# Performance work log

Hardware: AMD Instinct MI355X
Metric: run time of the kernel (lower is better)

The kernel has to match this reference:

```python
import jax, jax.numpy as jnp
import numpy as np
import math

V, H, NH, L, S, B = 100000, 2048, 64, 2, 512, 2
HD = H // NH  # 32
MAX_LEN = 5000
EPS_NORM = 1e-5
EPS_ATTN = 1e-6


def build_pe():
    # PositionalEncoding buffer: pe[max_len, 1, d_model]
    position = jnp.arange(MAX_LEN, dtype=jnp.float32)[:, None]
    div_term = jnp.exp(jnp.arange(0, H, 2, dtype=jnp.float32) * (-math.log(10000.0) / H))
    ang = position * div_term  # [max_len, H/2]
    pe = jnp.zeros((MAX_LEN, 1, H), dtype=jnp.float32)
    pe = pe.at[:, 0, 0::2].set(jnp.sin(ang))
    pe = pe.at[:, 0, 1::2].set(jnp.cos(ang))
    return pe


def fast_inv_sqrt(x):
    # Quake fast inverse sqrt; the bit-trick seed is detached in the original
    x2 = x * 0.5
    i = jax.lax.bitcast_convert_type(jax.lax.stop_gradient(x.astype(jnp.float32)), jnp.int32)
    i = jnp.int32(1597463007) - (i >> 1)
    y = jax.lax.bitcast_convert_type(i, jnp.float32)
    return y * (1.5 - x2 * y * y)  # grad flows only through x2, as in torch


def sr_norm(h, w, b):
    mean = h.mean(-1, keepdims=True)
    var = ((h - mean) ** 2).mean(-1, keepdims=True)  # biased variance
    inv = fast_inv_sqrt(var + EPS_NORM)
    return w * ((h - mean) * inv) + b


def attn_layer(x, wq, bq, wk, bk, wv, bv, wo, bo, nw, nb):
    # x: [B, S, H]; weights stored [in, out]
    def heads(t):
        return t.reshape(B, S, NH, HD).transpose(0, 2, 1, 3)  # [B, NH, S, HD]
    q = heads(x @ wq + bq)
    k = heads(x @ wk + bk)
    v = heads(x @ wv + bv)
    scores = jnp.einsum('bhqd,bhkd->bhqk', q, k) / math.sqrt(HD)
    a = jax.nn.softmax(scores, axis=-1)
    # dropout is identity in eval; then double softmax (exp/sum) + sigmoid gate
    e = jnp.exp(a)
    a2 = e / (e.sum(-1, keepdims=True) + EPS_ATTN)
    cw = a2 * jax.nn.sigmoid(a2)
    o = jnp.einsum('bhqk,bhkd->bhqd', cw, v)
    o = o.transpose(0, 2, 1, 3).reshape(B, S, H)
    o = o @ wo + bo
    return sr_norm(o + x, nw, nb)


def setup_inputs():
    key = jax.random.key(0)
    ks = jax.random.split(key, 12)
    def rn(k, shape):
        return jax.random.normal(k, shape, dtype=jnp.float32) * 0.02
    return {
        'src': jax.random.randint(ks[0], (B, S), 0, V),
        'emb': jax.random.uniform(ks[1], (V, H), minval=-0.1, maxval=0.1, dtype=jnp.float32),
        'Wq': rn(ks[2], (L, H, H)), 'bq': jnp.zeros((L, H), jnp.float32),
        'Wk': rn(ks[3], (L, H, H)), 'bk': jnp.zeros((L, H), jnp.float32),
        'Wv': rn(ks[4], (L, H, H)), 'bv': jnp.zeros((L, H), jnp.float32),
        'Wo': rn(ks[5], (L, H, H)), 'bo': jnp.zeros((L, H), jnp.float32),
        'nw': jnp.ones((L, H), jnp.float32), 'nb': jnp.zeros((L, H), jnp.float32),
        'Wout': jax.random.uniform(ks[6], (H, V), minval=-0.1, maxval=0.1, dtype=jnp.float32),
        'bout': jnp.zeros((V,), jnp.float32),
    }


def reference(src, emb, Wq, bq, Wk, bk, Wv, bv, Wo, bo, nw, nb, Wout, bout):
    x = emb[src] * math.sqrt(H)  # [B, S, H]
    pe = build_pe()
    # Faithful to pe[:x.size(0)] where x is [B, S, H]: indexes by BATCH dim
    x = x + pe[:x.shape[0]]  # [B, 1, H] broadcast over seq
    for l in range(L):
        x = attn_layer(x, Wq[l], bq[l], Wk[l], bk[l], Wv[l], bv[l],
                       Wo[l], bo[l], nw[l], nb[l])
    return x @ Wout + bout  # [B, S, V]
```

## Files before the change

### kernel.cpp

```cpp
#include <hip/hip_runtime.h>


#define DEVINL __device__ __forceinline__

typedef float f32x4 __attribute__((ext_vector_type(4)));
typedef __bf16 bf16x8 __attribute__((ext_vector_type(8)));
typedef __bf16 bf16x2v __attribute__((ext_vector_type(2)));

DEVINL unsigned int pk2(float a, float b) {
  bf16x2v v;
  v[0] = (__bf16)a;
  v[1] = (__bf16)b;
  return __builtin_bit_cast(unsigned int, v);
}

DEVINL void gload_lds16(const void* g, void* l) {
  __builtin_amdgcn_global_load_lds(
      (const __attribute__((address_space(1))) unsigned int*)g,
      (__attribute__((address_space(3))) unsigned int*)l, 16, 0, 0);
}

__global__ __launch_bounds__(256) void peinit_kernel(float* __restrict__ pe_tab) {
  const int h = blockIdx.x * 256 + threadIdx.x;
  const float c = -9.210340371976184f / 2048.f;
  const int i = h >> 1;
  const float dv = expf((float)(2 * i) * c);
#pragma unroll
  for (int b = 0; b < 2; ++b) {
    float ang = (float)b * dv;
    pe_tab[b * 2048 + h] = (h & 1) ? cosf(ang) : sinf(ang);
  }
}

__global__ __launch_bounds__(256) void embed_kernel(
    const int* __restrict__ src, const float* __restrict__ emb,
    const float* __restrict__ pe_tab, float* __restrict__ x, unsigned short* __restrict__ xbf) {
  const int row = blockIdx.x;
  const int b = row >> 9;
  const int tok = src[row];
  const float sqrtH = 45.25483399593904f;
  const float* er = emb + (size_t)tok * 2048;
  const float* pr = pe_tab + b * 2048;
  for (int c0 = threadIdx.x * 4; c0 < 2048; c0 += 1024) {
    float4 e = *(const float4*)(er + c0);
    float4 p = *(const float4*)(pr + c0);
    float r0 = fmaf(e.x, sqrtH, p.x), r1 = fmaf(e.y, sqrtH, p.y);
    float r2 = fmaf(e.z, sqrtH, p.z), r3 = fmaf(e.w, sqrtH, p.w);
    *(float4*)(x + (size_t)row * 2048 + c0) = make_float4(r0, r1, r2, r3);
    *(uint2*)&xbf[(size_t)row * 2048 + c0] = make_uint2(pk2(r0, r1), pk2(r2, r3));
  }
}

__global__ __launch_bounds__(256) void wtrans_kernel(
    const float* __restrict__ W, unsigned short* __restrict__ WT, const int N) {
  __shared__ float t[64][65];
  const int tid = threadIdx.x;
  const int n0 = blockIdx.x * 64, k0 = blockIdx.y * 64;
  const int c4 = (tid & 15) * 4;
#pragma unroll
  for (int it = 0; it < 4; ++it) {
    int kl = it * 16 + (tid >> 4);
    int n = n0 + c4;
    float4 wv;
    if (n + 3 < N) {
      wv = *(const float4*)(W + (size_t)(k0 + kl) * N + n);
    } else {
      wv.x = (n + 0 < N) ? W[(size_t)(k0 + kl) * N + n + 0] : 0.f;
      wv.y = (n + 1 < N) ? W[(size_t)(k0 + kl) * N + n + 1] : 0.f;
      wv.z = (n + 2 < N) ? W[(size_t)(k0 + kl) * N + n + 2] : 0.f;
      wv.w = (n + 3 < N) ? W[(size_t)(k0 + kl) * N + n + 3] : 0.f;
    }
    t[kl][c4 + 0] = wv.x;
    t[kl][c4 + 1] = wv.y;
    t[kl][c4 + 2] = wv.z;
    t[kl][c4 + 3] = wv.w;
  }
  __syncthreads();
  const int kp = (tid & 7) * 8;
#pragma unroll
  for (int j = 0; j < 2; ++j) {
    int nl = j * 32 + (tid >> 3);
    uint4 u;
    u.x = pk2(t[kp + 0][nl], t[kp + 1][nl]);
    u.y = pk2(t[kp + 2][nl], t[kp + 3][nl]);
    u.z = pk2(t[kp + 4][nl], t[kp + 5][nl]);
    u.w = pk2(t[kp + 6][nl], t[kp + 7][nl]);
    *(uint4*)&WT[(size_t)(n0 + nl) * 2048 + k0 + kp] = u;
  }
}

template <int BM, int NN>
DEVINL void gemm_bf_body(const unsigned short* __restrict__ A,
                         const unsigned short* __restrict__ BT,
                         const float* __restrict__ bias, float* __restrict__ C,
                         const int m0, const int n0) {
  constexpr int K = 2048;
  constexpr int NT = K / 32;
  constexpr int WM = BM / 32;
  constexpr int LP = BM / 64 + 2;
  __shared__ __align__(16) unsigned short A_lds[3][BM * 32];
  __shared__ __align__(16) unsigned short B_lds[3][128 * 32];

  const int tid = threadIdx.x;
  const int w = tid >> 6, lane = tid & 63;
  const int wm = w >> 1, wn = w & 1;

  const int aRow = lane >> 2;
  const int aChunk = (lane & 3) ^ ((lane >> 3) & 3);

  int aOff[WM], bOff[4];
#pragma unroll
  for (int mi = 0; mi < WM; ++mi) {
    int m = wm * (BM / 2) + mi * 16 + (lane & 15);
    aOff[mi] = m * 32 + ((lane >> 4) ^ ((m >> 1) & 3)) * 8;
  }
#pragma unroll
  for (int ni = 0; ni < 4; ++ni) {
    int n = wn * 64 + ni * 16 + (lane & 15);
    bOff[ni] = n * 32 + ((lane >> 4) ^ ((n >> 1) & 3)) * 8;
  }

  f32x4 acc[WM][4] = {};

  auto stage = [&](int k0, int bf) {
#pragma unroll
    for (int i = 0; i < BM / 64; ++i) {
      int r0 = (w * (BM / 64) + i) * 16;
      gload_lds16(A + (size_t)(m0 + r0 + aRow) * K + k0 + aChunk * 8, &A_lds[bf][r0 * 32]);
    }
#pragma unroll
    for (int i = 0; i < 2; ++i) {
      int r0 = (w * 2 + i) * 16;
      gload_lds16(BT + (size_t)(n0 + r0 + aRow) * K + k0 + aChunk * 8, &B_lds[bf][r0 * 32]);
    }
  };
  auto compute = [&](int bf) {
    bf16x8 af[WM], bfr[4];
#pragma unroll
    for (int mi = 0; mi < WM; ++mi) af[mi] = *(const bf16x8*)&A_lds[bf][aOff[mi]];
#pragma unroll
    for (int ni = 0; ni < 4; ++ni) bfr[ni] = *(const bf16x8*)&B_lds[bf][bOff[ni]];
#pragma unroll
    for (int mi = 0; mi < WM; ++mi)
#pragma unroll
      for (int ni = 0; ni < 4; ++ni)
        acc[mi][ni] = __builtin_amdgcn_mfma_f32_16x16x32_bf16(af[mi], bfr[ni], acc[mi][ni], 0, 0, 0);
  };

  stage(0, 0);
  stage(32, 1);
  for (int t = 0; t < NT - 1; ++t) {
    asm volatile("s_waitcnt vmcnt(%0)" :: "i"(LP) : "memory");
    __builtin_amdgcn_s_barrier();
    if (t < NT - 2) stage((t + 2) * 32, (t + 2) % 3);
    compute(t % 3);
  }
  asm volatile("s_waitcnt vmcnt(0)" ::: "memory");
  __builtin_amdgcn_s_barrier();
  compute((NT - 1) % 3);

  const int r0w = (lane >> 4) * 4;
  const int lrow = lane & 15;
#pragma unroll
  for (int mi = 0; mi < WM; ++mi)
#pragma unroll
    for (int ni = 0; ni < 4; ++ni) {
      int ccol = n0 + wn * 64 + ni * 16 + lrow;
      if ((NN % 128 == 0) || ccol < NN) {
        float bv = bias[ccol];
#pragma unroll
        for (int r = 0; r < 4; ++r) {
          int crow = m0 + wm * (BM / 2) + mi * 16 + r0w + r;
          C[(size_t)crow * NN + ccol] = acc[mi][ni][r] + bv;
        }
      }
    }
}

template <int BM, int NN>
__global__ __launch_bounds__(256) void gemm_bf_kernel(
    const unsigned short* __restrict__ A, const unsigned short* __restrict__ BT,
    const float* __restrict__ bias, float* __restrict__ C) {
  gemm_bf_body<BM, NN>(A, BT, bias, C, blockIdx.x * BM, blockIdx.y * 128);
}

__global__ __launch_bounds__(256) void gemm_qkv_bf_kernel(
    const unsigned short* __restrict__ A, const unsigned short* __restrict__ WT,
    const float* __restrict__ bq, const float* __restrict__ bk, const float* __restrict__ bv,
    float* __restrict__ q, float* __restrict__ k, float* __restrict__ v) {
  const int z = blockIdx.z;
  const unsigned short* BT = WT + (size_t)z * 2048 * 2048;
  const float* bias = (z == 0) ? bq : (z == 1) ? bk : bv;
  float* C = (z == 0) ? q : (z == 1) ? k : v;
  gemm_bf_body<128, 2048>(A, BT, bias, C, blockIdx.x * 128, blockIdx.y * 128);
}

__global__ __launch_bounds__(256) void gemm_final_bf_kernel(
    const unsigned short* __restrict__ A, const unsigned short* __restrict__ BT,
    const float* __restrict__ bias, float* __restrict__ C) {
  const int bid = blockIdx.x;
  const int f = (bid & 7) * (gridDim.x >> 3) + (bid >> 3);
  gemm_bf_body<128, 100000>(A, BT, bias, C, (f & 7) * 128, (f >> 3) * 128);
}

template <int BM>
DEVINL void gemm_body(const unsigned short* __restrict__ A, const float* __restrict__ B,
                      const float* __restrict__ bias, float* __restrict__ C,
                      const int N, const int m0, const int n0) {
  constexpr int K = 2048;
  constexpr int WM = BM / 32;
  constexpr int AI = BM / 64;
  __shared__ __align__(16) unsigned short A_lds[2][BM * 32];
  __shared__ __align__(16) unsigned short B_lds[2][128 * 32];

  const int tid = threadIdx.x;
  const int w = tid >> 6, lane = tid & 63;
  const int wm = w >> 1, wn = w & 1;

  const int n_local = tid & 127;
  const int kq = tid >> 7;
  const int col = n0 + n_local;
  const bool colok = col < N;
  const int bswz = (n_local >> 1) & 3;

  const int aRow = lane >> 2;
  const int aChunk = (lane & 3) ^ ((lane >> 3) & 3);

  int aOff[WM], bOff[4];
#pragma unroll
  for (int mi = 0; mi < WM; ++mi) {
    int m = wm * (BM / 2) + mi * 16 + (lane & 15);
    aOff[mi] = m * 32 + ((lane >> 4) ^ ((m >> 1) & 3)) * 8;
  }
#pragma unroll
  for (int ni = 0; ni < 4; ++ni) {
    int n = wn * 64 + ni * 16 + (lane & 15);
    bOff[ni] = n * 32 + ((lane >> 4) ^ ((n >> 1) & 3)) * 8;
  }

  f32x4 acc[WM][4] = {};
  float fB[16];

  auto stageA = [&](int k0, int bf) {
#pragma unroll
    for (int i = 0; i < AI; ++i) {
      int r0 = (w * AI + i) * 16;
      gload_lds16(A + (size_t)(m0 + r0 + aRow) * K + k0 + aChunk * 8, &A_lds[bf][r0 * 32]);
    }
  };
  auto loadB = [&](int k0) {
#pragma unroll
    for (int g = 0; g < 4; ++g) {
      int kl = (g * 2 + kq) * 4;
#pragma unroll
      for (int i = 0; i < 4; ++i)
        fB[g * 4 + i] = colok ? B[(size_t)(k0 + kl + i) * N + col] : 0.f;
    }
  };
  auto writeB = [&](int bf) {
#pragma unroll
    for (int g = 0; g < 4; ++g) {
      int kl = (g * 2 + kq) * 4;
      uint2 p = make_uint2(pk2(fB[g * 4 + 0], fB[g * 4 + 1]),
                           pk2(fB[g * 4 + 2], fB[g * 4 + 3]));
      int chunk = (kl >> 3) ^ bswz;
      *(uint2*)&B_lds[bf][n_local * 32 + chunk * 8 + (kl & 7)] = p;
    }
  };
  auto compute = [&](int bf) {
    bf16x8 af[WM], bfr[4];
#pragma unroll
    for (int mi = 0; mi < WM; ++mi) af[mi] = *(const bf16x8*)&A_lds[bf][aOff[mi]];
#pragma unroll
    for (int ni = 0; ni < 4; ++ni) bfr[ni] = *(const bf16x8*)&B_lds[bf][bOff[ni]];
#pragma unroll
    for (int mi = 0; mi < WM; ++mi)
#pragma unroll
      for (int ni = 0; ni < 4; ++ni)
        acc[mi][ni] = __builtin_amdgcn_mfma_f32_16x16x32_bf16(af[mi], bfr[ni], acc[mi][ni], 0, 0, 0);
  };

  stageA(0, 0);
  loadB(0);
  writeB(0);
  __syncthreads();
  int buf = 0;
  for (int t = 0; t < K / 32 - 1; ++t) {
    stageA((t + 1) * 32, buf ^ 1);
    loadB((t + 1) * 32);
    compute(buf);
    writeB(buf ^ 1);
    __syncthreads();
    buf ^= 1;
  }
  compute(buf);

  const int r0w = (lane >> 4) * 4;
  const int lrow = lane & 15;
#pragma unroll
  for (int mi = 0; mi < WM; ++mi)
#pragma unroll
    for (int ni = 0; ni < 4; ++ni) {
      int ccol = n0 + wn * 64 + ni * 16 + lrow;
      if (ccol < N) {
        float bv = bias[ccol];
#pragma unroll
        for (int r = 0; r < 4; ++r) {
          int crow = m0 + wm * (BM / 2) + mi * 16 + r0w + r;
          C[(size_t)crow * N + ccol] = acc[mi][ni][r] + bv;
        }
      }
    }
}

__global__ __launch_bounds__(256) void gemm_qkv_kernel(
    const unsigned short* __restrict__ A,
    const float* __restrict__ Wq, const float* __restrict__ Wk, const float* __restrict__ Wv,
    const float* __restrict__ bq, const float* __restrict__ bk, const float* __restrict__ bv,
    float* __restrict__ q, float* __restrict__ k, float* __restrict__ v) {
  const int z = blockIdx.z;
  const float* B = (z == 0) ? Wq : (z == 1) ? Wk : Wv;
  const float* bias = (z == 0) ? bq : (z == 1) ? bk : bv;
  float* C = (z == 0) ? q : (z == 1) ? k : v;
  gemm_body<64>(A, B, bias, C, 2048, blockIdx.x * 64, blockIdx.y * 128);
}

template <int BM>
__global__ __launch_bounds__(256) void gemm_kernel(
    const unsigned short* __restrict__ A, const float* __restrict__ B,
    const float* __restrict__ bias, float* __restrict__ C, const int N) {
  gemm_body<BM>(A, B, bias, C, N, blockIdx.x * BM, blockIdx.y * 128);
}

__global__ __launch_bounds__(256) void gemm_final_kernel(
    const unsigned short* __restrict__ A, const float* __restrict__ B,
    const float* __restrict__ bias, float* __restrict__ C, const int N) {
  const int bid = blockIdx.x;
  const int f = (bid & 7) * (gridDim.x >> 3) + (bid >> 3);
  gemm_body<128>(A, B, bias, C, N, (f & 7) * 128, (f >> 3) * 128);
}

__global__ __launch_bounds__(256) void attn_kernel(
    const float* __restrict__ q, const float* __restrict__ k,
    const float* __restrict__ v, unsigned short* __restrict__ o) {
  __shared__ __align__(16) float K_lds[512 * 32];
  const int tid = threadIdx.x;
  const int blk = blockIdx.x;
  const int bh = blk >> 2, chunk = blk & 3;
  const int b = bh >> 6, h = bh & 63;
  const size_t headoff = (size_t)b * 512 * 2048 + (size_t)h * 32;

  const float* kb = k + headoff;
#pragma unroll
  for (int i = 0; i < 16; ++i) {
    int flat = i * 256 + tid;
    int j = flat >> 3, d4 = flat & 7;
    *(float4*)&K_lds[j * 32 + d4 * 4] = *(const float4*)(kb + (size_t)j * 2048 + d4 * 4);
  }
  __syncthreads();

  const int row = chunk * 128 + (tid >> 1);
  const int half = tid & 1;
  const int j0 = half * 256, j1 = j0 + 256;
  const float* qr = q + headoff + (size_t)row * 2048;
  float4 Q[8];
#pragma unroll
  for (int d = 0; d < 8; ++d) Q[d] = *(const float4*)(qr + d * 4);

  const float scale = 0.17677669529663689f;
  auto dot = [&](int j) -> float {
    const float4* kr = (const float4*)&K_lds[j * 32];
    float p0 = 0.f, p1 = 0.f, p2 = 0.f, p3 = 0.f;
#pragma unroll
    for (int d = 0; d < 8; ++d) {
      float4 kk = kr[d];
      p0 = fmaf(Q[d].x, kk.x, p0);
      p1 = fmaf(Q[d].y, kk.y, p1);
      p2 = fmaf(Q[d].z, kk.z, p2);
      p3 = fmaf(Q[d].w, kk.w, p3);
    }
    return ((p0 + p1) + (p2 + p3)) * scale;
  };

  float m = -1e30f, denom = 0.f;
  for (int j = j0; j < j1; ++j) {
    float s = dot(j);
    float nm = fmaxf(m, s);
    denom = denom * __expf(m - nm) + __expf(s - nm);
    m = nm;
  }
  {
    float m2 = __shfl_xor(m, 1);
    float d2 = __shfl_xor(denom, 1);
    float mm = fmaxf(m, m2);
    denom = denom * __expf(m - mm) + d2 * __expf(m2 - mm);
    m = mm;
  }
  const float invd = 1.f / denom;

  float sum_e = 0.f;
  for (int j = j0; j < j1; ++j) {
    float a = __expf(dot(j) - m) * invd;
    sum_e += __expf(a);
  }
  sum_e += __shfl_xor(sum_e, 1);
  const float inv_se = 1.f / (sum_e + 1e-6f);

  float4 accv[8];
#pragma unroll
  for (int d = 0; d < 8; ++d) accv[d] = make_float4(0.f, 0.f, 0.f, 0.f);
  const float* vb = v + headoff;
  float4 vcur[8];
#pragma unroll
  for (int d = 0; d < 8; ++d) vcur[d] = *(const float4*)(vb + (size_t)j0 * 2048 + d * 4);
  for (int j = j0; j < j1; ++j) {
    float4 vnxt[8];
    if (j + 1 < j1) {
      const float4* vr = (const float4*)(vb + (size_t)(j + 1) * 2048);
#pragma unroll
      for (int d = 0; d < 8; ++d) vnxt[d] = vr[d];
    } else {
#pragma unroll
      for (int d = 0; d < 8; ++d) vnxt[d] = vcur[d];
    }
    float a = __expf(dot(j) - m) * invd;
    float e = __expf(a);
    float a2 = e * inv_se;
    float cw = a2 / (1.f + __expf(-a2));
#pragma unroll
    for (int d = 0; d < 8; ++d) {
      accv[d].x = fmaf(cw, vcur[d].x, accv[d].x);
      accv[d].y = fmaf(cw, vcur[d].y, accv[d].y);
      accv[d].z = fmaf(cw, vcur[d].z, accv[d].z);
      accv[d].w = fmaf(cw, vcur[d].w, accv[d].w);
    }
#pragma unroll
    for (int d = 0; d < 8; ++d) vcur[d] = vnxt[d];
  }
#pragma unroll
  for (int d = 0; d < 8; ++d) {
    accv[d].x += __shfl_xor(accv[d].x, 1);
    accv[d].y += __shfl_xor(accv[d].y, 1);
    accv[d].z += __shfl_xor(accv[d].z, 1);
    accv[d].w += __shfl_xor(accv[d].w, 1);
  }
  unsigned short* orow = o + headoff + (size_t)row * 2048;
#pragma unroll
  for (int g = 0; g < 4; ++g) {
    int d = half * 4 + g;
    uint2 p = make_uint2(pk2(accv[d].x, accv[d].y), pk2(accv[d].z, accv[d].w));
    *(uint2*)&orow[d * 4] = p;
  }
}

__global__ __launch_bounds__(256) void norm_kernel(
    const float* __restrict__ o, const float* __restrict__ xin,
    const float* __restrict__ w, const float* __restrict__ bb,
    float* __restrict__ xout, unsigned short* __restrict__ xbf) {
  __shared__ float red[4];
  const int row = blockIdx.x, tid = threadIdx.x;
  const float* op = o + (size_t)row * 2048;
  const float* xp = xin + (size_t)row * 2048;
  float4 hv[2];
#pragma unroll
  for (int i = 0; i < 2; ++i) {
    float4 a = *(const float4*)(op + tid * 4 + i * 1024);
    float4 c = *(const float4*)(xp + tid * 4 + i * 1024);
    hv[i] = make_float4(a.x + c.x, a.y + c.y, a.z + c.z, a.w + c.w);
  }
  float s = 0.f;
#pragma unroll
  for (int i = 0; i < 2; ++i) s += hv[i].x + hv[i].y + hv[i].z + hv[i].w;
  for (int off = 32; off; off >>= 1) s += __shfl_down(s, off);
  if ((tid & 63) == 0) red[tid >> 6] = s;
  __syncthreads();
  const float mean = (red[0] + red[1] + red[2] + red[3]) * (1.f / 2048.f);
  __syncthreads();

  float vs = 0.f;
#pragma unroll
  for (int i = 0; i < 2; ++i) {
    float dx = hv[i].x - mean, dy = hv[i].y - mean, dz = hv[i].z - mean, dw = hv[i].w - mean;
    vs += dx * dx + dy * dy + dz * dz + dw * dw;
  }
  for (int off = 32; off; off >>= 1) vs += __shfl_down(vs, off);
  if ((tid & 63) == 0) red[tid >> 6] = vs;
  __syncthreads();
  const float var = (red[0] + red[1] + red[2] + red[3]) * (1.f / 2048.f);

  const float xv = var + 1e-5f;
  int ii = __float_as_int(xv);
  ii = 1597463007 - (ii >> 1);
  float y = __int_as_float(ii);
  y = y * (1.5f - 0.5f * xv * y * y);

#pragma unroll
  for (int i = 0; i < 2; ++i) {
    int c0 = tid * 4 + i * 1024;
    float4 wv = *(const float4*)(w + c0);
    float4 bv = *(const float4*)(bb + c0);
    float r0 = wv.x * ((hv[i].x - mean) * y) + bv.x;
    float r1 = wv.y * ((hv[i].y - mean) * y) + bv.y;
    float r2 = wv.z * ((hv[i].z - mean) * y) + bv.z;
    float r3 = wv.w * ((hv[i].w - mean) * y) + bv.w;
    *(float4*)(xout + (size_t)row * 2048 + c0) = make_float4(r0, r1, r2, r3);
    *(uint2*)&xbf[(size_t)row * 2048 + c0] = make_uint2(pk2(r0, r1), pk2(r2, r3));
  }
}

extern "C" void kernel_launch(void* const* d_in, const int* in_sizes, int n_in,
                              void* d_out, int out_size, void* d_ws, size_t ws_size,
                              hipStream_t stream) {
  const int*   src  = (const int*)d_in[0];
  const float* emb  = (const float*)d_in[1];
  const float* Wq   = (const float*)d_in[2];
  const float* bq   = (const float*)d_in[3];
  const float* Wk   = (const float*)d_in[4];
  const float* bk   = (const float*)d_in[5];
  const float* Wv   = (const float*)d_in[6];
  const float* bv   = (const float*)d_in[7];
  const float* Wo   = (const float*)d_in[8];
  const float* bo   = (const float*)d_in[9];
  const float* nw   = (const float*)d_in[10];
  const float* nb   = (const float*)d_in[11];
  const float* Wout = (const float*)d_in[12];
  const float* bout = (const float*)d_in[13];
  float* out = (float*)d_out;

  char* ws = (char*)d_ws;
  float* x  = (float*)(ws);
  float* qb = (float*)(ws + (8ll << 20));
  float* kb = (float*)(ws + (16ll << 20));
  float* vb = (float*)(ws + (24ll << 20));
  float* ob = (float*)(ws + (32ll << 20));
  unsigned short* xbf = (unsigned short*)(ws + (40ll << 20));
  unsigned short* abf = (unsigned short*)(ws + (44ll << 20));
  float* pe_tab = ob;

  const unsigned long long NEED = (112ull << 20) + 100096ull * 2048ull * 2ull;
  const bool big = (unsigned long long)ws_size >= NEED;
  unsigned short* WTp = (unsigned short*)(ws + (48ll << 20));
  unsigned short* WTo = (unsigned short*)(ws + (112ll << 20));

  peinit_kernel<<<8, 256, 0, stream>>>(pe_tab);
  embed_kernel<<<1024, 256, 0, stream>>>(src, emb, pe_tab, x, xbf);

  if (big) {
    for (int l = 0; l < 2; ++l) {
      const size_t wo_ = (size_t)l * 2048 * 2048;
      const float* Wm[4] = {Wq + wo_, Wk + wo_, Wv + wo_, Wo + wo_};
      for (int mt = 0; mt < 4; ++mt)
        wtrans_kernel<<<dim3(32, 32), 256, 0, stream>>>(
            Wm[mt], WTp + (size_t)(l * 4 + mt) * 2048 * 2048, 2048);
    }
    wtrans_kernel<<<dim3(1564, 32), 256, 0, stream>>>(Wout, WTo, 100000);

    for (int l = 0; l < 2; ++l) {
      const size_t bo_ = (size_t)l * 2048;
      const unsigned short* WTl = WTp + (size_t)(l * 4) * 2048 * 2048;
      gemm_qkv_bf_kernel<<<dim3(8, 16, 3), 256, 0, stream>>>(
          xbf, WTl, bq + bo_, bk + bo_, bv + bo_, qb, kb, vb);
      attn_kernel<<<512, 256, 0, stream>>>(qb, kb, vb, abf);
      gemm_bf_kernel<64, 2048><<<dim3(16, 16), 256, 0, stream>>>(
          abf, WTl + (size_t)3 * 2048 * 2048, bo + bo_, ob);
      norm_kernel<<<1024, 256, 0, stream>>>(ob, x, nw + bo_, nb + bo_, x, xbf);
    }
    gemm_final_bf_kernel<<<8 * 782, 256, 0, stream>>>(xbf, WTo, bout, out);
  } else {
    for (int l = 0; l < 2; ++l) {
      const size_t wo_ = (size_t)l * 2048 * 2048;
      const size_t bo_ = (size_t)l * 2048;
      gemm_qkv_kernel<<<dim3(16, 16, 3), 256, 0, stream>>>(
          xbf, Wq + wo_, Wk + wo_, Wv + wo_, bq + bo_, bk + bo_, bv + bo_, qb, kb, vb);
      attn_kernel<<<512, 256, 0, stream>>>(qb, kb, vb, abf);
      gemm_kernel<64><<<dim3(16, 16), 256, 0, stream>>>(abf, Wo + wo_, bo + bo_, ob, 2048);
      norm_kernel<<<1024, 256, 0, stream>>>(ob, x, nw + bo_, nb + bo_, x, xbf);
    }
    gemm_final_kernel<<<8 * 782, 256, 0, stream>>>(xbf, Wout, bout, out, 100000);
  }
}
```

Before: 1.957 ms.

## Merge weight transposes, use double-buffered GEMM, split attention rows four ways

Several changes at once. The eight per-layer weight-transpose launches become one batched launch. The bf16 GEMM moves from a three-stage LDS pipeline with a partial vmcnt wait to a simpler double-buffered loop that syncs fully every step. The attention kernel splits each query row over four threads instead of two, doubling the block count. The Wo projection now uses BM=128 tiles. Launch overhead drops and attention gets more parallelism, but the GEMM loses some load/compute overlap and Wo gets fewer blocks.

After: 2.328 ms. 1.19x slower.

```diff
diff --git a/kernel.cpp b/kernel.cpp
--- a/kernel.cpp
+++ b/kernel.cpp
@@ -51,11 +51,10 @@
   }
 }
 
-__global__ __launch_bounds__(256) void wtrans_kernel(
-    const float* __restrict__ W, unsigned short* __restrict__ WT, const int N) {
+DEVINL void wtrans_body(const float* __restrict__ W, unsigned short* __restrict__ WT,
+                        const int N, const int n0, const int k0) {
   __shared__ float t[64][65];
   const int tid = threadIdx.x;
-  const int n0 = blockIdx.x * 64, k0 = blockIdx.y * 64;
   const int c4 = (tid & 15) * 4;
 #pragma unroll
   for (int it = 0; it < 4; ++it) {
@@ -89,17 +88,30 @@
   }
 }
 
+__global__ __launch_bounds__(256) void wtrans_kernel(
+    const float* __restrict__ W, unsigned short* __restrict__ WT, const int N) {
+  wtrans_body(W, WT, N, blockIdx.x * 64, blockIdx.y * 64);
+}
+
+__global__ __launch_bounds__(256) void wtrans8_kernel(
+    const float* __restrict__ Wq, const float* __restrict__ Wk,
+    const float* __restrict__ Wv, const float* __restrict__ Wo,
+    unsigned short* __restrict__ WTp) {
+  const int z = blockIdx.z, l = z >> 2, mt = z & 3;
+  const float* Wm = (mt == 0) ? Wq : (mt == 1) ? Wk : (mt == 2) ? Wv : Wo;
+  wtrans_body(Wm + (size_t)l * 2048 * 2048,
+              WTp + (size_t)z * 2048 * 2048, 2048, blockIdx.x * 64, blockIdx.y * 64);
+}
+
 template <int BM, int NN>
 DEVINL void gemm_bf_body(const unsigned short* __restrict__ A,
                          const unsigned short* __restrict__ BT,
                          const float* __restrict__ bias, float* __restrict__ C,
                          const int m0, const int n0) {
   constexpr int K = 2048;
-  constexpr int NT = K / 32;
   constexpr int WM = BM / 32;
-  constexpr int LP = BM / 64 + 2;
-  __shared__ __align__(16) unsigned short A_lds[3][BM * 32];
-  __shared__ __align__(16) unsigned short B_lds[3][128 * 32];
+  __shared__ __align__(16) unsigned short A_lds[2][BM * 32];
+  __shared__ __align__(16) unsigned short B_lds[2][128 * 32];
 
   const int tid = threadIdx.x;
   const int w = tid >> 6, lane = tid & 63;
@@ -148,16 +160,15 @@
   };
 
   stage(0, 0);
-  stage(32, 1);
-  for (int t = 0; t < NT - 1; ++t) {
-    asm volatile("s_waitcnt vmcnt(%0)" :: "i"(LP) : "memory");
-    __builtin_amdgcn_s_barrier();
-    if (t < NT - 2) stage((t + 2) * 32, (t + 2) % 3);
-    compute(t % 3);
-  }
-  asm volatile("s_waitcnt vmcnt(0)" ::: "memory");
-  __builtin_amdgcn_s_barrier();
-  compute((NT - 1) % 3);
+  __syncthreads();
+  int buf = 0;
+  for (int t = 0; t < K / 32 - 1; ++t) {
+    stage((t + 1) * 32, buf ^ 1);
+    compute(buf);
+    __syncthreads();
+    buf ^= 1;
+  }
+  compute(buf);
 
   const int r0w = (lane >> 4) * 4;
   const int lrow = lane & 15;
@@ -346,7 +357,7 @@
   __shared__ __align__(16) float K_lds[512 * 32];
   const int tid = threadIdx.x;
   const int blk = blockIdx.x;
-  const int bh = blk >> 2, chunk = blk & 3;
+  const int bh = blk >> 3, chunk = blk & 7;
   const int b = bh >> 6, h = bh & 63;
   const size_t headoff = (size_t)b * 512 * 2048 + (size_t)h * 32;
 
@@ -359,9 +370,9 @@
   }
   __syncthreads();
 
-  const int row = chunk * 128 + (tid >> 1);
-  const int half = tid & 1;
-  const int j0 = half * 256, j1 = j0 + 256;
+  const int row = chunk * 64 + (tid >> 2);
+  const int qtr = tid & 3;
+  const int j0 = qtr * 128, j1 = j0 + 128;
   const float* qr = q + headoff + (size_t)row * 2048;
   float4 Q[8];
 #pragma unroll
@@ -389,9 +400,10 @@
     denom = denom * __expf(m - nm) + __expf(s - nm);
     m = nm;
   }
-  {
-    float m2 = __shfl_xor(m, 1);
-    float d2 = __shfl_xor(denom, 1);
+#pragma unroll
+  for (int off = 1; off <= 2; off <<= 1) {
+    float m2 = __shfl_xor(m, off);
+    float d2 = __shfl_xor(denom, off);
     float mm = fmaxf(m, m2);
     denom = denom * __expf(m - mm) + d2 * __expf(m2 - mm);
     m = mm;
@@ -404,6 +416,7 @@
     sum_e += __expf(a);
   }
   sum_e += __shfl_xor(sum_e, 1);
+  sum_e += __shfl_xor(sum_e, 2);
   const float inv_se = 1.f / (sum_e + 1e-6f);
 
   float4 accv[8];
@@ -443,11 +456,15 @@
     accv[d].y += __shfl_xor(accv[d].y, 1);
     accv[d].z += __shfl_xor(accv[d].z, 1);
     accv[d].w += __shfl_xor(accv[d].w, 1);
+    accv[d].x += __shfl_xor(accv[d].x, 2);
+    accv[d].y += __shfl_xor(accv[d].y, 2);
+    accv[d].z += __shfl_xor(accv[d].z, 2);
+    accv[d].w += __shfl_xor(accv[d].w, 2);
   }
   unsigned short* orow = o + headoff + (size_t)row * 2048;
 #pragma unroll
-  for (int g = 0; g < 4; ++g) {
-    int d = half * 4 + g;
+  for (int g = 0; g < 2; ++g) {
+    int d = qtr * 2 + g;
     uint2 p = make_uint2(pk2(accv[d].x, accv[d].y), pk2(accv[d].z, accv[d].w));
     *(uint2*)&orow[d * 4] = p;
   }
@@ -546,13 +563,7 @@
   embed_kernel<<<1024, 256, 0, stream>>>(src, emb, pe_tab, x, xbf);
 
   if (big) {
-    for (int l = 0; l < 2; ++l) {
-      const size_t wo_ = (size_t)l * 2048 * 2048;
-      const float* Wm[4] = {Wq + wo_, Wk + wo_, Wv + wo_, Wo + wo_};
-      for (int mt = 0; mt < 4; ++mt)
-        wtrans_kernel<<<dim3(32, 32), 256, 0, stream>>>(
-            Wm[mt], WTp + (size_t)(l * 4 + mt) * 2048 * 2048, 2048);
-    }
+    wtrans8_kernel<<<dim3(32, 32, 8), 256, 0, stream>>>(Wq, Wk, Wv, Wo, WTp);
     wtrans_kernel<<<dim3(1564, 32), 256, 0, stream>>>(Wout, WTo, 100000);
 
     for (int l = 0; l < 2; ++l) {
@@ -560,8 +571,8 @@
       const unsigned short* WTl = WTp + (size_t)(l * 4) * 2048 * 2048;
       gemm_qkv_bf_kernel<<<dim3(8, 16, 3), 256, 0, stream>>>(
           xbf, WTl, bq + bo_, bk + bo_, bv + bo_, qb, kb, vb);
-      attn_kernel<<<512, 256, 0, stream>>>(qb, kb, vb, abf);
-      gemm_bf_kernel<64, 2048><<<dim3(16, 16), 256, 0, stream>>>(
+      attn_kernel<<<1024, 256, 0, stream>>>(qb, kb, vb, abf);
+      gemm_bf_kernel<128, 2048><<<dim3(8, 16), 256, 0, stream>>>(
           abf, WTl + (size_t)3 * 2048 * 2048, bo + bo_, ob);
       norm_kernel<<<1024, 256, 0, stream>>>(ob, x, nw + bo_, nb + bo_, x, xbf);
     }
@@ -572,7 +583,7 @@
       const size_t bo_ = (size_t)l * 2048;
       gemm_qkv_kernel<<<dim3(16, 16, 3), 256, 0, stream>>>(
           xbf, Wq + wo_, Wk + wo_, Wv + wo_, bq + bo_, bk + bo_, bv + bo_, qb, kb, vb);
-      attn_kernel<<<512, 256, 0, stream>>>(qb, kb, vb, abf);
+      attn_kernel<<<1024, 256, 0, stream>>>(qb, kb, vb, abf);
       gemm_kernel<64><<<dim3(16, 16), 256, 0, stream>>>(abf, Wo + wo_, bo + bo_, ob, 2048);
       norm_kernel<<<1024, 256, 0, stream>>>(ob, x, nw + bo_, nb + bo_, x, xbf);
     }
```
